# Kernel tuning notes

Measured on AMD Instinct MI355X. Metric: run time of the kernel, lower is better.

## Reference

```python
import jax, jax.numpy as jnp
import numpy as np

B, G = 2, 8192
IMG_H, IMG_W = 256, 256
CHUNK = 64  # gaussians composited per scan step


def setup_inputs() -> dict:
    key = jax.random.key(0)
    ks = jax.random.split(key, 7)
    # means inside the image
    means2d = jax.random.uniform(ks[0], (B, G, 2), dtype=jnp.float32) * jnp.array([IMG_W, IMG_H], jnp.float32)
    # positive-definite conic (inverse 2D covariance): a, b, c with a,c>0 and b^2 < a*c
    a = jax.random.uniform(ks[1], (B, G), jnp.float32, 0.02, 0.25)
    c = jax.random.uniform(ks[2], (B, G), jnp.float32, 0.02, 0.25)
    b = (jax.random.uniform(ks[3], (B, G), jnp.float32) * 2.0 - 1.0) * 0.5 * jnp.sqrt(a * c)
    conics = jnp.stack([a, b, c], axis=-1)
    colors = jax.random.uniform(ks[4], (B, G, 3), dtype=jnp.float32)
    opacities = jax.random.uniform(ks[5], (B, G), jnp.float32, 0.05, 1.0)
    depths = jax.random.uniform(ks[6], (B, G), jnp.float32, 0.1, 10.0)
    return {"means2d": means2d, "conics": conics, "colors": colors,
            "opacities": opacities, "depths": depths,
            "image_height": IMG_H, "image_width": IMG_W}


def _rasterize(means2d, conics, colors, opacities, order, Hh, Ww):
    """Front-to-back alpha compositing of depth-ordered 2D Gaussians.

    Mathematically identical to the tile-binned/per-tile-sorted kernel: the
    tiling is only a scheduling decomposition of global depth-ordered
    over-compositing.
    """
    Bb, Gg = opacities.shape
    P = Hh * Ww
    # gather in front-to-back depth order
    gm = jnp.take_along_axis(means2d, order[..., None], axis=1)   # [B,G,2]
    gc = jnp.take_along_axis(conics, order[..., None], axis=1)    # [B,G,3]
    gl = jnp.take_along_axis(colors, order[..., None], axis=1)    # [B,G,3]
    go = jnp.take_along_axis(opacities, order, axis=1)            # [B,G]

    ys = jnp.arange(Hh, dtype=jnp.float32) + 0.5
    xs = jnp.arange(Ww, dtype=jnp.float32) + 0.5
    gy, gx = jnp.meshgrid(ys, xs, indexing='ij')
    pxf = gx.reshape(-1)  # [P]
    pyf = gy.reshape(-1)  # [P]

    n_chunks = Gg // CHUNK
    gm = gm.reshape(Bb, n_chunks, CHUNK, 2).transpose(1, 0, 2, 3)
    gc = gc.reshape(Bb, n_chunks, CHUNK, 3).transpose(1, 0, 2, 3)
    gl = gl.reshape(Bb, n_chunks, CHUNK, 3).transpose(1, 0, 2, 3)
    go = go.reshape(Bb, n_chunks, CHUNK).transpose(1, 0, 2)

    def step(carry, ch):
        img, T = carry                      # [B,P,3], [B,P] transmittance
        m, cn, cl, op = ch
        dx = pxf[None, None, :] - m[..., 0:1]   # [B,C,P]
        dy = pyf[None, None, :] - m[..., 1:2]
        a = cn[..., 0:1]
        b = cn[..., 1:2]
        c = cn[..., 2:3]
        power = -0.5 * (a * dx * dx + c * dy * dy) - b * dx * dy
        alpha = op[..., None] * jnp.exp(jnp.minimum(power, 0.0))
        alpha = jnp.minimum(alpha, 0.999)
        alpha = jnp.where(alpha < 1.0 / 255.0, 0.0, alpha)      # kernel skip-threshold
        Tc = jnp.cumprod(1.0 - alpha, axis=1)                   # within-chunk transmittance
        Tb = T[:, None, :] * jnp.concatenate(
            [jnp.ones_like(Tc[:, :1]), Tc[:, :-1]], axis=1)     # exclusive product
        img = img + jnp.einsum('bcp,bcd->bpd', Tb * alpha, cl)
        T = T * Tc[:, -1, :]
        return (img, T), None

    init = (jnp.zeros((Bb, P, 3), jnp.float32), jnp.ones((Bb, P), jnp.float32))
    (img, T), _ = jax.lax.scan(step, init, (gm, gc, gl, go))
    return img.reshape(Bb, Hh, Ww, 3), (1.0 - T).reshape(Bb, Hh, Ww)


def reference(means2d, conics, colors, opacities, depths, image_height, image_width):
    order = jnp.argsort(depths, axis=1)  # front-to-back
    image, alpha = _rasterize(means2d, conics, colors, opacities, order,
                              int(image_height), int(image_width))
    return image, alpha
```

## Files before the change

kernel.cpp:

```cpp
#include <hip/hip_runtime.h>
#include <hip/hip_fp16.h>
#include <stdint.h>

#define GCOUNT 8192
#define BATCH 2
#define IMGH 256
#define IMGW 256
#define TILE 16
#define TILES_X (IMGW / TILE)
#define TILES_Y (IMGH / TILE)
#define MAXLIST 1024

#define LDS_BAR() do { asm volatile("s_waitcnt lgkmcnt(0)" ::: "memory"); \
                       __builtin_amdgcn_s_barrier(); } while (0)

__global__ __launch_bounds__(256) void prep(
    const float* __restrict__ means, const float* __restrict__ conics,
    const float* __restrict__ colors, const float* __restrict__ opac,
    const float* __restrict__ depths,
    float4* __restrict__ gdat,
    uint32_t* __restrict__ gbbox,
    unsigned long long* __restrict__ gkey)
{
    const int t = blockIdx.x * 256 + threadIdx.x;
    if (t >= BATCH * GCOUNT) return;
    const int g = t & (GCOUNT - 1);

    const float mx  = means[t * 2 + 0];
    const float my  = means[t * 2 + 1];
    const float ca  = conics[t * 3 + 0];
    const float cb  = conics[t * 3 + 1];
    const float cc  = conics[t * 3 + 2];
    const float cr  = colors[t * 3 + 0];
    const float cg  = colors[t * 3 + 1];
    const float cbl = colors[t * 3 + 2];
    const float op  = opac[t];
    const float dep = depths[t];

    const float lop = __logf(op);
    const float tt  = lop + 5.5412635f;
    const float det = ca * cc - cb * cb;
    const float inv = 2.0f * tt / det;
    const float dxm = sqrtf(inv * cc) + 1.0f;
    const float dym = sqrtf(inv * ca) + 1.0f;

    int x0 = max(0, (int)floorf((mx - dxm) * (1.0f / TILE)));
    int x1 = min(TILES_X - 1, (int)floorf((mx + dxm) * (1.0f / TILE)));
    int y0 = max(0, (int)floorf((my - dym) * (1.0f / TILE)));
    int y1 = min(TILES_Y - 1, (int)floorf((my + dym) * (1.0f / TILE)));
    uint32_t bb;
    if (x1 < x0 || y1 < y0)
        bb = 0xFFu;
    else
        bb = (uint32_t)x0 | ((uint32_t)x1 << 8) |
             ((uint32_t)y0 << 16) | ((uint32_t)y1 << 24);

    const __half hr = __float2half_rn(cr);
    const __half hg = __float2half_rn(cg);
    const uint32_t pk = ((uint32_t)__half_as_ushort(hg) << 16) |
                        (uint32_t)__half_as_ushort(hr);

    gdat[t * 2 + 0] = make_float4(mx, my, -0.5f * ca, -cb);
    gdat[t * 2 + 1] = make_float4(-0.5f * cc, lop, __uint_as_float(pk), cbl);
    gbbox[t] = bb;
    gkey[t]  = ((unsigned long long)__float_as_uint(dep) << 13) | (unsigned)g;
}

__global__ __launch_bounds__(1024, 8) void raster(
    const float4* __restrict__ gdat, const uint32_t* __restrict__ gbbox,
    const unsigned long long* __restrict__ gkey, float* __restrict__ out)
{
    __shared__ unsigned long long keys[MAXLIST];
    __shared__ float4 sdat[MAXLIST][2];
    __shared__ uint16_t sinv[MAXLIST];
    __shared__ float4 xch[8][64][4];
    __shared__ int scnt;

    const int tid  = threadIdx.x;
    const int lane = tid & 63;
    const int wid  = tid >> 6;
    const int tx = blockIdx.x, ty = blockIdx.y, b = blockIdx.z;
    const int bg = b * GCOUNT;

    if (tid == 0) scnt = 0;
    LDS_BAR();

    const unsigned long long mlt = (1ull << lane) - 1ull;
    {
        uint32_t v[8];
#pragma unroll
        for (int k = 0; k < 8; ++k)
            v[k] = gbbox[bg + k * 1024 + tid];
        bool hit[8];
        unsigned long long bal[8];
        int cnts[8], sum = 0;
#pragma unroll
        for (int k = 0; k < 8; ++k) {
            const int x0 = v[k] & 0xFF, x1 = (v[k] >> 8) & 0xFF;
            const int y0 = (v[k] >> 16) & 0xFF, y1 = (v[k] >> 24) & 0xFF;
            hit[k] = (tx >= x0) & (tx <= x1) & (ty >= y0) & (ty <= y1);
            bal[k] = __ballot(hit[k]);
            cnts[k] = __popcll(bal[k]);
            sum += cnts[k];
        }
        int wbase = 0;
        if (lane == 0 && sum) wbase = atomicAdd(&scnt, sum);
        wbase = __shfl(wbase, 0);
#pragma unroll
        for (int k = 0; k < 8; ++k) {
            if (hit[k]) {
                const int pos = wbase + __popcll(bal[k] & mlt);
                if (pos < MAXLIST)
                    keys[pos] = (gkey[bg + k * 1024 + tid] << 10) | (unsigned)pos;
            }
            wbase += cnts[k];
        }
    }
    LDS_BAR();
    const int cnt = min(scnt, MAXLIST);

    const bool h0 = tid < cnt;
    float4 r0a, r0b;
    if (h0) {
        const int g0 = (int)((keys[tid] >> 10) & 8191);
        r0a = gdat[(bg + g0) * 2 + 0];
        r0b = gdat[(bg + g0) * 2 + 1];
    }

    int P = 64;
    while (P < cnt) P <<= 1;
    for (int i = cnt + tid; i < P; i += 1024) keys[i] = ~0ull;
    LDS_BAR();

    if ((wid << 6) < P) {
        unsigned long long key = keys[(wid << 6) | lane];
        const bool descBlock = (wid & 1);
#pragma unroll
        for (int k = 2; k <= 64; k <<= 1) {
            for (int j = k >> 1; j > 0; j >>= 1) {
                const unsigned long long other = __shfl_xor(key, j);
                const bool asc   = (((lane & k) == 0) != descBlock);
                const bool lower = ((lane & j) == 0);
                const unsigned long long mn = (key < other) ? key : other;
                const unsigned long long mx = (key < other) ? other : key;
                key = (asc == lower) ? mn : mx;
            }
        }
        keys[(wid << 6) | lane] = key;
    }
    LDS_BAR();

    for (int k = 128; k <= P; k <<= 1) {
        for (int j = k >> 1; j >= 64; j >>= 1) {
            const int i = tid;
            if (i < P) {
                const int ixj = i ^ j;
                if (ixj > i) {
                    const unsigned long long A = keys[i], Bv = keys[ixj];
                    const bool asc = ((i & k) == 0);
                    if ((A > Bv) == asc) { keys[i] = Bv; keys[ixj] = A; }
                }
            }
            LDS_BAR();
        }
        if ((wid << 6) < P) {
            const int base = wid << 6;
            unsigned long long key = keys[base | lane];
            const bool asc = ((base & k) == 0);
#pragma unroll
            for (int j = 32; j > 0; j >>= 1) {
                const unsigned long long other = __shfl_xor(key, j);
                const bool lower = ((lane & j) == 0);
                const unsigned long long mn = (key < other) ? key : other;
                const unsigned long long mx = (key < other) ? other : key;
                key = (asc == lower) ? mn : mx;
            }
            keys[base | lane] = key;
        }
        LDS_BAR();
    }

    for (int i = tid; i < cnt; i += 1024)
        sinv[(int)(keys[i] & 1023u)] = (uint16_t)i;
    LDS_BAR();
    if (h0) {
        const int q = sinv[tid];
        sdat[q][0] = r0a;
        sdat[q][1] = r0b;
    }
    LDS_BAR();

    const int px0 = tx * TILE + ((lane & 3) << 2);
    const int py  = ty * TILE + (lane >> 2);
    const float pxf = px0 + 0.5f, pyf = py + 0.5f;
    const int lo = (cnt * wid) >> 4;
    const int hi = (cnt * (wid + 1)) >> 4;

    float T0 = 1.f, cr0 = 0.f, cg0 = 0.f, cb0 = 0.f;
    float T1 = 1.f, cr1 = 0.f, cg1 = 0.f, cb1 = 0.f;
    float T2 = 1.f, cr2 = 0.f, cg2 = 0.f, cb2 = 0.f;
    float T3 = 1.f, cr3 = 0.f, cg3 = 0.f, cb3 = 0.f;

    for (int s = lo; s < hi; ++s) {
        const float4 A = sdat[s][0];
        const float4 Bv = sdat[s][1];
        const float dx = pxf - A.x, dy = pyf - A.y;
        const float qbdy = A.w * dy;
        float pw0 = fmaf(A.z * dx, dx, Bv.y);
        pw0 = fmaf(Bv.x * dy, dy, pw0);
        pw0 = fmaf(qbdy, dx, pw0);
        const float qa2 = A.z + A.z;
        float stp = fmaf(qa2, dx, qbdy) + A.z;
        const float pw1 = pw0 + stp;  stp += qa2;
        const float pw2 = pw1 + stp;  stp += qa2;
        const float pw3 = pw2 + stp;

        const uint32_t pk = __float_as_uint(Bv.z);
        const float gr = __half2float(__ushort_as_half((unsigned short)(pk & 0xFFFFu)));
        const float gg = __half2float(__ushort_as_half((unsigned short)(pk >> 16)));
        const float gb = Bv.w;

        float a0 = fminf(__expf(pw0), 0.999f); a0 = (a0 < (1.f/255.f)) ? 0.f : a0;
        float a1 = fminf(__expf(pw1), 0.999f); a1 = (a1 < (1.f/255.f)) ? 0.f : a1;
        float a2 = fminf(__expf(pw2), 0.999f); a2 = (a2 < (1.f/255.f)) ? 0.f : a2;
        float a3 = fminf(__expf(pw3), 0.999f); a3 = (a3 < (1.f/255.f)) ? 0.f : a3;

        const float w0 = T0 * a0; cr0 = fmaf(w0, gr, cr0); cg0 = fmaf(w0, gg, cg0); cb0 = fmaf(w0, gb, cb0); T0 -= w0;
        const float w1 = T1 * a1; cr1 = fmaf(w1, gr, cr1); cg1 = fmaf(w1, gg, cg1); cb1 = fmaf(w1, gb, cb1); T1 -= w1;
        const float w2 = T2 * a2; cr2 = fmaf(w2, gr, cr2); cg2 = fmaf(w2, gg, cg2); cb2 = fmaf(w2, gb, cb2); T2 -= w2;
        const float w3 = T3 * a3; cr3 = fmaf(w3, gr, cr3); cg3 = fmaf(w3, gg, cg3); cb3 = fmaf(w3, gb, cb3); T3 -= w3;
    }

    int ls = 0;
    for (int st = 1; st < 16; st <<= 1, ++ls) {
        const int m = (st << 1) - 1;
        if ((wid & m) == st) {
            const int slot = wid >> (ls + 1);
            xch[slot][lane][0] = make_float4(cr0, cg0, cb0, T0);
            xch[slot][lane][1] = make_float4(cr1, cg1, cb1, T1);
            xch[slot][lane][2] = make_float4(cr2, cg2, cb2, T2);
            xch[slot][lane][3] = make_float4(cr3, cg3, cb3, T3);
        }
        LDS_BAR();
        if ((wid & m) == 0) {
            const int slot = wid >> (ls + 1);
            float4 e;
            e = xch[slot][lane][0]; cr0 = fmaf(T0, e.x, cr0); cg0 = fmaf(T0, e.y, cg0); cb0 = fmaf(T0, e.z, cb0); T0 *= e.w;
            e = xch[slot][lane][1]; cr1 = fmaf(T1, e.x, cr1); cg1 = fmaf(T1, e.y, cg1); cb1 = fmaf(T1, e.z, cb1); T1 *= e.w;
            e = xch[slot][lane][2]; cr2 = fmaf(T2, e.x, cr2); cg2 = fmaf(T2, e.y, cg2); cb2 = fmaf(T2, e.z, cb2); T2 *= e.w;
            e = xch[slot][lane][3]; cr3 = fmaf(T3, e.x, cr3); cg3 = fmaf(T3, e.y, cg3); cb3 = fmaf(T3, e.z, cb3); T3 *= e.w;
        }
        LDS_BAR();
    }

    if (wid == 0) {
        const int pix0 = (b * IMGH + py) * IMGW + px0;
        float* o = out + (size_t)pix0 * 3;
        *(float4*)(o + 0) = make_float4(cr0, cg0, cb0, cr1);
        *(float4*)(o + 4) = make_float4(cg1, cb1, cr2, cg2);
        *(float4*)(o + 8) = make_float4(cb2, cr3, cg3, cb3);
        *(float4*)&out[(size_t)BATCH * IMGH * IMGW * 3 + pix0] =
            make_float4(1.f - T0, 1.f - T1, 1.f - T2, 1.f - T3);
    }
}

extern "C" void kernel_launch(void* const* d_in, const int* in_sizes, int n_in,
                              void* d_out, int out_size, void* d_ws, size_t ws_size,
                              hipStream_t stream) {
    const float* means  = (const float*)d_in[0];
    const float* conics = (const float*)d_in[1];
    const float* colors = (const float*)d_in[2];
    const float* opac   = (const float*)d_in[3];
    const float* depths = (const float*)d_in[4];

    char* ws = (char*)d_ws;
    const size_t NG = (size_t)BATCH * GCOUNT;
    float4*             gdat  = (float4*)ws;
    uint32_t*           gbbox = (uint32_t*)(ws + NG * 32);
    unsigned long long* gkey  = (unsigned long long*)(ws + NG * 36);
    float* out = (float*)d_out;

    hipLaunchKernelGGL(prep, dim3((BATCH * GCOUNT + 255) / 256), dim3(256), 0, stream,
                       means, conics, colors, opac, depths, gdat, gbbox, gkey);
    hipLaunchKernelGGL(raster, dim3(TILES_X, TILES_Y, BATCH), dim3(1024), 0, stream,
                       gdat, gbbox, gkey, out);
}
```

Measured before the change: 29.26 us.

## Cull gaussian-tile pairs with exact ellipse-rectangle test via per-gaussian tile mask

Result: slower. 31.20 us (+6.6%).

```diff
diff --git a/kernel.cpp b/kernel.cpp
--- a/kernel.cpp
+++ b/kernel.cpp
@@ -20,7 +20,8 @@
     const float* __restrict__ depths,
     float4* __restrict__ gdat,
     uint32_t* __restrict__ gbbox,
-    unsigned long long* __restrict__ gkey)
+    unsigned long long* __restrict__ gkey,
+    unsigned long long* __restrict__ gmask)
 {
     const int t = blockIdx.x * 256 + threadIdx.x;
     if (t >= BATCH * GCOUNT) return;
@@ -44,31 +45,61 @@
     const float dxm = sqrtf(inv * cc) + 1.0f;
     const float dym = sqrtf(inv * ca) + 1.0f;
 
-    int x0 = max(0, (int)floorf((mx - dxm) * (1.0f / TILE)));
-    int x1 = min(TILES_X - 1, (int)floorf((mx + dxm) * (1.0f / TILE)));
-    int y0 = max(0, (int)floorf((my - dym) * (1.0f / TILE)));
-    int y1 = min(TILES_Y - 1, (int)floorf((my + dym) * (1.0f / TILE)));
-    uint32_t bb;
-    if (x1 < x0 || y1 < y0)
-        bb = 0xFFu;
-    else
-        bb = (uint32_t)x0 | ((uint32_t)x1 << 8) |
-             ((uint32_t)y0 << 16) | ((uint32_t)y1 << 24);
+    const int x0 = max(0, (int)floorf((mx - dxm) * (1.0f / TILE)));
+    const int x1 = min(TILES_X - 1, (int)floorf((mx + dxm) * (1.0f / TILE)));
+    const int y0 = max(0, (int)floorf((my - dym) * (1.0f / TILE)));
+    const int y1 = min(TILES_Y - 1, (int)floorf((my + dym) * (1.0f / TILE)));
+
+    uint32_t bb = 0xFFu;
+    unsigned long long mask = 0ull;
+    if (x1 >= x0 && y1 >= y0) {
+        const float thr = tt + 1e-3f;
+        for (int tyi = y0; tyi <= y1; ++tyi) {
+            const float ly = tyi * (float)TILE + 0.5f - my;
+            const float hy = ly + (float)(TILE - 1);
+            for (int txi = x0; txi <= x1; ++txi) {
+                const float lx = txi * (float)TILE + 0.5f - mx;
+                const float hx = lx + (float)(TILE - 1);
+                bool keep;
+                if (lx <= 0.f && 0.f <= hx && ly <= 0.f && 0.f <= hy) {
+                    keep = true;
+                } else {
+                    float mF;
+                    float dys = fminf(fmaxf(-cb * lx / cc, ly), hy);
+                    mF = 0.5f * ca * lx * lx + cb * lx * dys + 0.5f * cc * dys * dys;
+                    dys = fminf(fmaxf(-cb * hx / cc, ly), hy);
+                    mF = fminf(mF, 0.5f * ca * hx * hx + cb * hx * dys + 0.5f * cc * dys * dys);
+                    float dxs = fminf(fmaxf(-cb * ly / ca, lx), hx);
+                    mF = fminf(mF, 0.5f * cc * ly * ly + cb * ly * dxs + 0.5f * ca * dxs * dxs);
+                    dxs = fminf(fmaxf(-cb * hy / ca, lx), hx);
+                    mF = fminf(mF, 0.5f * cc * hy * hy + cb * hy * dxs + 0.5f * ca * dxs * dxs);
+                    keep = (mF <= thr);
+                }
+                if (keep) mask |= 1ull << ((tyi - y0) * 8 + (txi - x0));
+            }
+        }
+        if (mask)
+            bb = (uint32_t)x0 | ((uint32_t)x1 << 8) |
+                 ((uint32_t)y0 << 16) | ((uint32_t)y1 << 24);
+    }
 
     const __half hr = __float2half_rn(cr);
     const __half hg = __float2half_rn(cg);
     const uint32_t pk = ((uint32_t)__half_as_ushort(hg) << 16) |
                         (uint32_t)__half_as_ushort(hr);
+    const float lop_c = fminf(lop, -0.0010005f);
 
     gdat[t * 2 + 0] = make_float4(mx, my, -0.5f * ca, -cb);
-    gdat[t * 2 + 1] = make_float4(-0.5f * cc, lop, __uint_as_float(pk), cbl);
+    gdat[t * 2 + 1] = make_float4(-0.5f * cc, lop_c, __uint_as_float(pk), cbl);
     gbbox[t] = bb;
+    gmask[t] = mask;
     gkey[t]  = ((unsigned long long)__float_as_uint(dep) << 13) | (unsigned)g;
 }
 
 __global__ __launch_bounds__(1024, 8) void raster(
     const float4* __restrict__ gdat, const uint32_t* __restrict__ gbbox,
-    const unsigned long long* __restrict__ gkey, float* __restrict__ out)
+    const unsigned long long* __restrict__ gkey,
+    const unsigned long long* __restrict__ gmask, float* __restrict__ out)
 {
     __shared__ unsigned long long keys[MAXLIST];
     __shared__ float4 sdat[MAXLIST][2];
@@ -86,19 +117,32 @@
     LDS_BAR();
 
     const unsigned long long mlt = (1ull << lane) - 1ull;
-    {
-        uint32_t v[8];
-#pragma unroll
-        for (int k = 0; k < 8; ++k)
-            v[k] = gbbox[bg + k * 1024 + tid];
-        bool hit[8];
-        unsigned long long bal[8];
-        int cnts[8], sum = 0;
-#pragma unroll
-        for (int k = 0; k < 8; ++k) {
+    for (int pass = 0; pass < 2; ++pass) {
+        const int base0 = pass * 4096;
+        uint32_t v[4];
+#pragma unroll
+        for (int k = 0; k < 4; ++k)
+            v[k] = gbbox[bg + base0 + k * 1024 + tid];
+        bool hit0[4];
+        int bx0[4], by0[4];
+#pragma unroll
+        for (int k = 0; k < 4; ++k) {
             const int x0 = v[k] & 0xFF, x1 = (v[k] >> 8) & 0xFF;
             const int y0 = (v[k] >> 16) & 0xFF, y1 = (v[k] >> 24) & 0xFF;
-            hit[k] = (tx >= x0) & (tx <= x1) & (ty >= y0) & (ty <= y1);
+            hit0[k] = (tx >= x0) & (tx <= x1) & (ty >= y0) & (ty <= y1);
+            bx0[k] = x0; by0[k] = y0;
+        }
+        unsigned long long mk[4];
+#pragma unroll
+        for (int k = 0; k < 4; ++k)
+            if (hit0[k]) mk[k] = gmask[bg + base0 + k * 1024 + tid];
+        bool hit[4];
+        unsigned long long bal[4];
+        int cnts[4], sum = 0;
+#pragma unroll
+        for (int k = 0; k < 4; ++k) {
+            hit[k] = hit0[k] &&
+                ((mk[k] >> ((ty - by0[k]) * 8 + (tx - bx0[k]))) & 1ull);
             bal[k] = __ballot(hit[k]);
             cnts[k] = __popcll(bal[k]);
             sum += cnts[k];
@@ -107,11 +151,11 @@
         if (lane == 0 && sum) wbase = atomicAdd(&scnt, sum);
         wbase = __shfl(wbase, 0);
 #pragma unroll
-        for (int k = 0; k < 8; ++k) {
+        for (int k = 0; k < 4; ++k) {
             if (hit[k]) {
                 const int pos = wbase + __popcll(bal[k] & mlt);
                 if (pos < MAXLIST)
-                    keys[pos] = (gkey[bg + k * 1024 + tid] << 10) | (unsigned)pos;
+                    keys[pos] = (gkey[bg + base0 + k * 1024 + tid] << 10) | (unsigned)pos;
             }
             wbase += cnts[k];
         }
@@ -201,6 +245,7 @@
     float T2 = 1.f, cr2 = 0.f, cg2 = 0.f, cb2 = 0.f;
     float T3 = 1.f, cr3 = 0.f, cg3 = 0.f, cb3 = 0.f;
 
+#pragma unroll 2
     for (int s = lo; s < hi; ++s) {
         const float4 A = sdat[s][0];
         const float4 Bv = sdat[s][1];
@@ -220,10 +265,10 @@
         const float gg = __half2float(__ushort_as_half((unsigned short)(pk >> 16)));
         const float gb = Bv.w;
 
-        float a0 = fminf(__expf(pw0), 0.999f); a0 = (a0 < (1.f/255.f)) ? 0.f : a0;
-        float a1 = fminf(__expf(pw1), 0.999f); a1 = (a1 < (1.f/255.f)) ? 0.f : a1;
-        float a2 = fminf(__expf(pw2), 0.999f); a2 = (a2 < (1.f/255.f)) ? 0.f : a2;
-        float a3 = fminf(__expf(pw3), 0.999f); a3 = (a3 < (1.f/255.f)) ? 0.f : a3;
+        const float a0 = (pw0 < -5.5412636f) ? 0.f : __expf(pw0);
+        const float a1 = (pw1 < -5.5412636f) ? 0.f : __expf(pw1);
+        const float a2 = (pw2 < -5.5412636f) ? 0.f : __expf(pw2);
+        const float a3 = (pw3 < -5.5412636f) ? 0.f : __expf(pw3);
 
         const float w0 = T0 * a0; cr0 = fmaf(w0, gr, cr0); cg0 = fmaf(w0, gg, cg0); cb0 = fmaf(w0, gb, cb0); T0 -= w0;
         const float w1 = T1 * a1; cr1 = fmaf(w1, gr, cr1); cg1 = fmaf(w1, gg, cg1); cb1 = fmaf(w1, gb, cb1); T1 -= w1;
@@ -278,10 +323,11 @@
     float4*             gdat  = (float4*)ws;
     uint32_t*           gbbox = (uint32_t*)(ws + NG * 32);
     unsigned long long* gkey  = (unsigned long long*)(ws + NG * 36);
+    unsigned long long* gmask = (unsigned long long*)(ws + NG * 44);
     float* out = (float*)d_out;
 
     hipLaunchKernelGGL(prep, dim3((BATCH * GCOUNT + 255) / 256), dim3(256), 0, stream,
-                       means, conics, colors, opac, depths, gdat, gbbox, gkey);
+                       means, conics, colors, opac, depths, gdat, gbbox, gkey, gmask);
     hipLaunchKernelGGL(raster, dim3(TILES_X, TILES_Y, BATCH), dim3(1024), 0, stream,
-                       gdat, gbbox, gkey, out);
+                       gdat, gbbox, gkey, gmask, out);
 }
```

## Flatten cross-wave merge, alias LDS buffers, and fold alpha clamp into prep

Applied to the files above, without the earlier changes.

New measurement: 33.81 us. +15.6%, slower.

```diff
diff --git a/kernel.cpp b/kernel.cpp
--- a/kernel.cpp
+++ b/kernel.cpp
@@ -59,9 +59,10 @@
     const __half hg = __float2half_rn(cg);
     const uint32_t pk = ((uint32_t)__half_as_ushort(hg) << 16) |
                         (uint32_t)__half_as_ushort(hr);
+    const float lop_c = fminf(lop, -0.0010005f);
 
     gdat[t * 2 + 0] = make_float4(mx, my, -0.5f * ca, -cb);
-    gdat[t * 2 + 1] = make_float4(-0.5f * cc, lop, __uint_as_float(pk), cbl);
+    gdat[t * 2 + 1] = make_float4(-0.5f * cc, lop_c, __uint_as_float(pk), cbl);
     gbbox[t] = bb;
     gkey[t]  = ((unsigned long long)__float_as_uint(dep) << 13) | (unsigned)g;
 }
@@ -70,11 +71,12 @@
     const float4* __restrict__ gdat, const uint32_t* __restrict__ gbbox,
     const unsigned long long* __restrict__ gkey, float* __restrict__ out)
 {
-    __shared__ unsigned long long keys[MAXLIST];
-    __shared__ float4 sdat[MAXLIST][2];
-    __shared__ uint16_t sinv[MAXLIST];
-    __shared__ float4 xch[8][64][4];
+    __shared__ __align__(16) char smem[61440];
     __shared__ int scnt;
+    unsigned long long* keys = (unsigned long long*)smem;
+    float4 (*sdat)[2] = (float4(*)[2])(smem + 8192);
+    uint16_t* sinv = (uint16_t*)(smem + 40960);
+    float4* xch = (float4*)smem;
 
     const int tid  = threadIdx.x;
     const int lane = tid & 63;
@@ -201,6 +203,7 @@
     float T2 = 1.f, cr2 = 0.f, cg2 = 0.f, cb2 = 0.f;
     float T3 = 1.f, cr3 = 0.f, cg3 = 0.f, cb3 = 0.f;
 
+#pragma unroll 2
     for (int s = lo; s < hi; ++s) {
         const float4 A = sdat[s][0];
         const float4 Bv = sdat[s][1];
@@ -220,10 +223,10 @@
         const float gg = __half2float(__ushort_as_half((unsigned short)(pk >> 16)));
         const float gb = Bv.w;
 
-        float a0 = fminf(__expf(pw0), 0.999f); a0 = (a0 < (1.f/255.f)) ? 0.f : a0;
-        float a1 = fminf(__expf(pw1), 0.999f); a1 = (a1 < (1.f/255.f)) ? 0.f : a1;
-        float a2 = fminf(__expf(pw2), 0.999f); a2 = (a2 < (1.f/255.f)) ? 0.f : a2;
-        float a3 = fminf(__expf(pw3), 0.999f); a3 = (a3 < (1.f/255.f)) ? 0.f : a3;
+        const float a0 = (pw0 < -5.5412636f) ? 0.f : __expf(pw0);
+        const float a1 = (pw1 < -5.5412636f) ? 0.f : __expf(pw1);
+        const float a2 = (pw2 < -5.5412636f) ? 0.f : __expf(pw2);
+        const float a3 = (pw3 < -5.5412636f) ? 0.f : __expf(pw3);
 
         const float w0 = T0 * a0; cr0 = fmaf(w0, gr, cr0); cg0 = fmaf(w0, gg, cg0); cb0 = fmaf(w0, gb, cb0); T0 -= w0;
         const float w1 = T1 * a1; cr1 = fmaf(w1, gr, cr1); cg1 = fmaf(w1, gg, cg1); cb1 = fmaf(w1, gb, cb1); T1 -= w1;
@@ -231,29 +234,24 @@
         const float w3 = T3 * a3; cr3 = fmaf(w3, gr, cr3); cg3 = fmaf(w3, gg, cg3); cb3 = fmaf(w3, gb, cb3); T3 -= w3;
     }
 
-    int ls = 0;
-    for (int st = 1; st < 16; st <<= 1, ++ls) {
-        const int m = (st << 1) - 1;
-        if ((wid & m) == st) {
-            const int slot = wid >> (ls + 1);
-            xch[slot][lane][0] = make_float4(cr0, cg0, cb0, T0);
-            xch[slot][lane][1] = make_float4(cr1, cg1, cb1, T1);
-            xch[slot][lane][2] = make_float4(cr2, cg2, cb2, T2);
-            xch[slot][lane][3] = make_float4(cr3, cg3, cb3, T3);
-        }
-        LDS_BAR();
-        if ((wid & m) == 0) {
-            const int slot = wid >> (ls + 1);
+    LDS_BAR();
+    if (wid) {
+        float4* dst = xch + ((wid - 1) << 8) + (lane << 2);
+        dst[0] = make_float4(cr0, cg0, cb0, T0);
+        dst[1] = make_float4(cr1, cg1, cb1, T1);
+        dst[2] = make_float4(cr2, cg2, cb2, T2);
+        dst[3] = make_float4(cr3, cg3, cb3, T3);
+    }
+    LDS_BAR();
+    if (wid == 0) {
+        for (int q = 0; q < 15; ++q) {
+            const float4* src = xch + (q << 8) + (lane << 2);
             float4 e;
-            e = xch[slot][lane][0]; cr0 = fmaf(T0, e.x, cr0); cg0 = fmaf(T0, e.y, cg0); cb0 = fmaf(T0, e.z, cb0); T0 *= e.w;
-            e = xch[slot][lane][1]; cr1 = fmaf(T1, e.x, cr1); cg1 = fmaf(T1, e.y, cg1); cb1 = fmaf(T1, e.z, cb1); T1 *= e.w;
-            e = xch[slot][lane][2]; cr2 = fmaf(T2, e.x, cr2); cg2 = fmaf(T2, e.y, cg2); cb2 = fmaf(T2, e.z, cb2); T2 *= e.w;
-            e = xch[slot][lane][3]; cr3 = fmaf(T3, e.x, cr3); cg3 = fmaf(T3, e.y, cg3); cb3 = fmaf(T3, e.z, cb3); T3 *= e.w;
-        }
-        LDS_BAR();
-    }
-
-    if (wid == 0) {
+            e = src[0]; cr0 = fmaf(T0, e.x, cr0); cg0 = fmaf(T0, e.y, cg0); cb0 = fmaf(T0, e.z, cb0); T0 *= e.w;
+            e = src[1]; cr1 = fmaf(T1, e.x, cr1); cg1 = fmaf(T1, e.y, cg1); cb1 = fmaf(T1, e.z, cb1); T1 *= e.w;
+            e = src[2]; cr2 = fmaf(T2, e.x, cr2); cg2 = fmaf(T2, e.y, cg2); cb2 = fmaf(T2, e.z, cb2); T2 *= e.w;
+            e = src[3]; cr3 = fmaf(T3, e.x, cr3); cg3 = fmaf(T3, e.y, cg3); cb3 = fmaf(T3, e.z, cb3); T3 *= e.w;
+        }
         const int pix0 = (b * IMGH + py) * IMGW + px0;
         float* o = out + (size_t)pix0 * 3;
         *(float4*)(o + 0) = make_float4(cr0, cg0, cb0, cr1);
```
